# Kernel tuning notes

Hardware: AMD Instinct MI355X
Metric: run time of the kernel (lower is better)

Reference implementation:

```python
import jax, jax.numpy as jnp
import numpy as np

HEADS = 4
DIM_HEAD = 64
INNER = HEADS * DIM_HEAD  # 256
MAP_SIZE = (8, 8, 8)
DN = ('NCDHW', 'OIDHW', 'NCDHW')


def _depthwise3d(x, w):
    # x: [B,C,D,H,W], w: [C,1,3,3,3] (torch groups=C layout)
    return jax.lax.conv_general_dilated(
        x, w, window_strides=(1, 1, 1), padding='SAME',
        dimension_numbers=DN, feature_group_count=x.shape[1])


def _dws_conv(x, dw, pw):
    # depthwise 3x3x3 then pointwise 1x1x1 (pw: [out,in])
    y = _depthwise3d(x, dw)
    return jnp.einsum('bcdhw,oc->bodhw', y, pw)


def _split_heads(t):
    # 'b (dim_head heads) d h w -> b heads (d h w) dim_head'
    B, C, D, H, W = t.shape
    t = t.reshape(B, DIM_HEAD, HEADS, D * H * W)
    return t.transpose(0, 2, 3, 1)


def _merge_heads(t, D, H, W):
    # 'b heads n dim_head -> b (dim_head heads) d h w'
    B = t.shape[0]
    return t.transpose(0, 3, 1, 2).reshape(B, DIM_HEAD * HEADS, D, H, W)


def setup_inputs() -> dict:
    key = jax.random.key(0)
    ks = jax.random.split(key, 8)
    B, feat_dim, map_dim, out_dim = 2, 128, 64, 128
    D = H = W = 24
    s = 0.02
    return {
        'feat': jax.random.normal(ks[0], (B, feat_dim, D, H, W), jnp.float32),
        'smap': jax.random.normal(ks[1], (B, map_dim) + MAP_SIZE, jnp.float32),
        'feat_qv_dw': jax.random.normal(ks[2], (feat_dim, 1, 3, 3, 3), jnp.float32) * s,
        'feat_qv_pw': jax.random.normal(ks[3], (2 * INNER, feat_dim), jnp.float32) * s,
        'feat_out_dw': jax.random.normal(ks[4], (INNER, 1, 3, 3, 3), jnp.float32) * s,
        'feat_out_pw': jax.random.normal(ks[5], (out_dim, INNER), jnp.float32) * s,
        'map_qv_w': jax.random.normal(ks[6], (2 * INNER, map_dim), jnp.float32) * s,
        'map_out_w': jax.random.normal(ks[7], (map_dim, INNER), jnp.float32) * s,
    }


def reference(feat, smap, feat_qv_dw, feat_qv_pw, feat_out_dw, feat_out_pw,
              map_qv_w, map_out_w):
    B, C, D, H, W = feat.shape
    scale = DIM_HEAD ** -0.5

    # projections
    fqv = _dws_conv(feat, feat_qv_dw, feat_qv_pw)           # [B, 2*inner, D,H,W]
    feat_q, feat_v = jnp.split(fqv, 2, axis=1)
    mqv = jnp.einsum('bcdhw,oc->bodhw', smap, map_qv_w)     # [B, 2*inner, 8,8,8]
    map_q, map_v = jnp.split(mqv, 2, axis=1)

    feat_q, feat_v = _split_heads(feat_q), _split_heads(feat_v)  # [B,h,N,dh]
    map_q, map_v = _split_heads(map_q), _split_heads(map_v)      # [B,h,M,dh]

    # shared scores, dual-direction softmax
    attn = jnp.einsum('bhid,bhjd->bhij', feat_q, map_q) * scale  # [B,h,N,M]
    feat_map_attn = jax.nn.softmax(attn, axis=-1)
    map_feat_attn = jax.nn.softmax(attn, axis=-2)

    feat_out = jnp.einsum('bhij,bhjd->bhid', feat_map_attn, map_v)   # [B,h,N,dh]
    map_out = jnp.einsum('bhji,bhjd->bhid', map_feat_attn, feat_v)   # [B,h,M,dh]

    feat_out = _merge_heads(feat_out, D, H, W)
    map_out = _merge_heads(map_out, *MAP_SIZE)

    feat_out = _dws_conv(feat_out, feat_out_dw, feat_out_pw)   # [B,out_dim,D,H,W]
    map_out = jnp.einsum('bcdhw,oc->bodhw', map_out, map_out_w)  # [B,map_dim,8,8,8]
    return feat_out, map_out
```

## Files before the change

### kernel.cpp

```cpp
#include <hip/hip_runtime.h>

#define BB 2
#define CH_FEAT 128
#define HEADS 4
#define DH 64
#define INNER 256
#define NPOS 13824
#define MPOS 512
#define DSZ 24
#define JSPLIT 12
#define JCHUNK (NPOS / JSPLIT)

typedef __attribute__((ext_vector_type(8))) short bf16x8;
typedef __attribute__((ext_vector_type(4))) float f32x4;

__device__ inline unsigned short bf16_rn(float x) {
  unsigned u = __builtin_bit_cast(unsigned, x);
  u += 0x7FFF + ((u >> 16) & 1);
  return (unsigned short)(u >> 16);
}
__device__ inline unsigned pk_bf16(float a, float b) {
  return (unsigned)bf16_rn(a) | ((unsigned)bf16_rn(b) << 16);
}
__device__ inline float4 ld_bf4(const unsigned short* p) {
  uint2 u = *(const uint2*)p;
  float4 f;
  f.x = __builtin_bit_cast(float, (u.x & 0xFFFFu) << 16);
  f.y = __builtin_bit_cast(float, u.x & 0xFFFF0000u);
  f.z = __builtin_bit_cast(float, (u.y & 0xFFFFu) << 16);
  f.w = __builtin_bit_cast(float, u.y & 0xFFFF0000u);
  return f;
}
__device__ inline void st_bf4(unsigned short* p, float4 v) {
  uint2 u;
  u.x = pk_bf16(v.x, v.y);
  u.y = pk_bf16(v.z, v.w);
  *(uint2*)p = u;
}

#define GL2LDS(g, l)                                                        \
  __builtin_amdgcn_global_load_lds(                                         \
      (const __attribute__((address_space(1))) void*)(g),                   \
      (__attribute__((address_space(3))) void*)(l), 16, 0, 0)

__device__ inline bf16x8 lds_frag(const char* tile, int row, int colb) {
  return *(const bf16x8*)(tile + row * 128 + (colb ^ ((row & 7) << 4)));
}
__device__ inline bf16x8 lds_fragP(const char* tile, int row, int colb, int pitch) {
  return *(const bf16x8*)(tile + row * pitch + (colb ^ ((row & 7) << 4)));
}

__global__ __launch_bounds__(512) void k_map_qv(const float* __restrict__ smap,
                                                const float* __restrict__ w,
                                                unsigned short* __restrict__ mapqb,
                                                unsigned short* __restrict__ mapvTb) {
  int bm = blockIdx.x;
  int b = bm >> 9, m = bm & 511;
  __shared__ float s[64];
  int t = threadIdx.x;
  if (t < 64) s[t] = smap[(size_t)(b * 64 + t) * MPOS + m];
  __syncthreads();
  const float* wr = w + t * 64;
  float acc = 0.f;
#pragma unroll
  for (int c = 0; c < 64; ++c) acc += wr[c] * s[c];
  int qv = t >> 8, c2 = t & 255, head = c2 & 3, dh = c2 >> 2;
  int bh = b * HEADS + head;
  if (qv == 0)
    mapqb[((size_t)bh * MPOS + m) * 64 + dh] = bf16_rn(acc * 0.125f);
  else
    mapvTb[((size_t)bh * 64 + dh) * MPOS + m] = bf16_rn(acc);
}

__global__ __launch_bounds__(576) void k_dw_f2b(const float* __restrict__ in,
                                                const float* __restrict__ w,
                                                unsigned short* __restrict__ out, int C) {
  int t = threadIdx.x;
  int bc = blockIdx.x;
  int c = bc & (C - 1), b = bc / C;
  int y = t % 24, z = t / 24;
  const float* wr = w + c * 27;
  const float* ip = in + (size_t)bc * NPOS;

  float wm[9][3];
  int off[9];
#pragma unroll
  for (int dz = 0; dz < 3; ++dz)
#pragma unroll
    for (int dy = 0; dy < 3; ++dy) {
      int r = dz * 3 + dy;
      int zz = z + dz - 1, yy = y + dy - 1;
      float m = ((unsigned)zz < 24u && (unsigned)yy < 24u) ? 1.f : 0.f;
      wm[r][0] = wr[dz * 9 + dy * 3 + 0] * m;
      wm[r][1] = wr[dz * 9 + dy * 3 + 1] * m;
      wm[r][2] = wr[dz * 9 + dy * 3 + 2] * m;
      int zc = min(max(zz, 0), 23), yc = min(max(yy, 0), 23);
      off[r] = (zc * 24 + yc) * 24;
    }

  float4 cur[9], nxt[9];
  float pl[9];
#pragma unroll
  for (int r = 0; r < 9; ++r) {
    pl[r] = 0.f;
    cur[r] = *(const float4*)(ip + off[r]);
    nxt[r] = *(const float4*)(ip + off[r] + 4);
  }

  unsigned short* op = out + ((size_t)b * C + c) * NPOS + (z * 24 + y) * 24;
#pragma unroll
  for (int xc = 0; xc < 6; ++xc) {
    float4 acc;
    acc.x = acc.y = acc.z = acc.w = 0.f;
#pragma unroll
    for (int r = 0; r < 9; ++r) {
      float w0 = wm[r][0], w1 = wm[r][1], w2 = wm[r][2];
      float4 cu = cur[r];
      acc.x += w0 * pl[r] + w1 * cu.x + w2 * cu.y;
      acc.y += w0 * cu.x + w1 * cu.y + w2 * cu.z;
      acc.z += w0 * cu.y + w1 * cu.z + w2 * cu.w;
      acc.w += w0 * cu.z + w1 * cu.w + w2 * nxt[r].x;
    }
    st_bf4(op + xc * 4, acc);
    if (xc < 5) {
#pragma unroll
      for (int r = 0; r < 9; ++r) {
        pl[r] = cur[r].w;
        cur[r] = nxt[r];
        nxt[r] = (xc < 4) ? *(const float4*)(ip + off[r] + (xc + 2) * 4)
                          : make_float4(0.f, 0.f, 0.f, 0.f);
      }
    }
  }
}

__global__ __launch_bounds__(576) void k_dw_b2b(const unsigned short* __restrict__ in,
                                                const float* __restrict__ w,
                                                unsigned short* __restrict__ out, int C) {
  int t = threadIdx.x;
  int bc = blockIdx.x;
  int c = bc & (C - 1), b = bc / C;
  int cm = (c & 63) * 4 + (c >> 6);
  int y = t % 24, z = t / 24;
  const float* wr = w + cm * 27;
  const unsigned short* ip = in + (size_t)bc * NPOS;

  float wm[9][3];
  int off[9];
#pragma unroll
  for (int dz = 0; dz < 3; ++dz)
#pragma unroll
    for (int dy = 0; dy < 3; ++dy) {
      int r = dz * 3 + dy;
      int zz = z + dz - 1, yy = y + dy - 1;
      float m = ((unsigned)zz < 24u && (unsigned)yy < 24u) ? 1.f : 0.f;
      wm[r][0] = wr[dz * 9 + dy * 3 + 0] * m;
      wm[r][1] = wr[dz * 9 + dy * 3 + 1] * m;
      wm[r][2] = wr[dz * 9 + dy * 3 + 2] * m;
      int zc = min(max(zz, 0), 23), yc = min(max(yy, 0), 23);
      off[r] = (zc * 24 + yc) * 24;
    }

  float4 cur[9], nxt[9];
  float pl[9];
#pragma unroll
  for (int r = 0; r < 9; ++r) {
    pl[r] = 0.f;
    cur[r] = ld_bf4(ip + off[r]);
    nxt[r] = ld_bf4(ip + off[r] + 4);
  }

  unsigned short* op = out + ((size_t)b * C + cm) * NPOS + (z * 24 + y) * 24;
#pragma unroll
  for (int xc = 0; xc < 6; ++xc) {
    float4 acc;
    acc.x = acc.y = acc.z = acc.w = 0.f;
#pragma unroll
    for (int r = 0; r < 9; ++r) {
      float w0 = wm[r][0], w1 = wm[r][1], w2 = wm[r][2];
      float4 cu = cur[r];
      acc.x += w0 * pl[r] + w1 * cu.x + w2 * cu.y;
      acc.y += w0 * cu.x + w1 * cu.y + w2 * cu.z;
      acc.z += w0 * cu.y + w1 * cu.z + w2 * cu.w;
      acc.w += w0 * cu.z + w1 * cu.w + w2 * nxt[r].x;
    }
    st_bf4(op + xc * 4, acc);
    if (xc < 5) {
#pragma unroll
      for (int r = 0; r < 9; ++r) {
        pl[r] = cur[r].w;
        cur[r] = nxt[r];
        nxt[r] = (xc < 4) ? ld_bf4(ip + off[r] + (xc + 2) * 4)
                          : make_float4(0.f, 0.f, 0.f, 0.f);
      }
    }
  }
}

__global__ __launch_bounds__(256) void k_trb(const unsigned short* __restrict__ in,
                                             unsigned short* __restrict__ outT, int C) {
  __shared__ unsigned sT[64][33];
  int t = threadIdx.x;
  int n0 = blockIdx.x * 64, c0 = blockIdx.y * 64, b = blockIdx.z;
  {
    int r = t >> 2, s8 = (t & 3) * 8;
    const unsigned short* ip = in + ((size_t)b * C + c0 + r) * NPOS + n0 + s8 * 2;
    uint4 a = *(const uint4*)(ip);
    uint4 b2 = *(const uint4*)(ip + 8);
    sT[r][s8 + 0] = a.x; sT[r][s8 + 1] = a.y; sT[r][s8 + 2] = a.z; sT[r][s8 + 3] = a.w;
    sT[r][s8 + 4] = b2.x; sT[r][s8 + 5] = b2.y; sT[r][s8 + 6] = b2.z; sT[r][s8 + 7] = b2.w;
  }
  __syncthreads();
  int nr = t >> 2, cs = (t & 3) * 16;
  int n2 = nr >> 1, nl = (nr & 1) * 16;
  unsigned pkv[8];
#pragma unroll
  for (int i = 0; i < 8; ++i) {
    unsigned lo = (sT[cs + 2 * i][n2] >> nl) & 0xFFFFu;
    unsigned hi = (sT[cs + 2 * i + 1][n2] >> nl) & 0xFFFFu;
    pkv[i] = lo | (hi << 16);
  }
  unsigned short* op = outT + ((size_t)b * NPOS + n0 + nr) * C + c0 + cs;
  *(uint4*)(op) = *(uint4*)&pkv[0];
  *(uint4*)(op + 8) = *(uint4*)&pkv[4];
}

__global__ __launch_bounds__(256) void k_pwqv_m(const unsigned short* __restrict__ dwtT,
                                                const float* __restrict__ pw,
                                                unsigned short* __restrict__ fqb,
                                                unsigned short* __restrict__ fvTb) {
  __shared__ __align__(16) char sAB[49152];
  char* sW = sAB;
  char* sB = sAB + 16384;
  int t = threadIdx.x, wave = t >> 6, lane = t & 63, g = lane >> 4, c = lane & 15;
  int n0 = blockIdx.x * 128, ti = blockIdx.y, b = blockIdx.z;
  int qv = ti >> 2, head = ti & 3, bh = b * 4 + head;

  {
    int r = t >> 2, ks = (t & 3) * 32;
    int co = qv * 256 + r * 4 + head;
    const float* wp = pw + (size_t)co * 128 + ks;
    unsigned pkv[16];
#pragma unroll
    for (int i = 0; i < 8; ++i) {
      float4 v = *(const float4*)(wp + i * 4);
      pkv[2 * i] = pk_bf16(v.x, v.y);
      pkv[2 * i + 1] = pk_bf16(v.z, v.w);
    }
#pragma unroll
    for (int u = 0; u < 4; ++u) {
      int colb = (ks * 2 + u * 16) ^ ((r & 7) << 4);
      *(uint4*)(sW + r * 256 + colb) = *(uint4*)&pkv[u * 4];
    }
  }
  const char* Bg = (const char*)(dwtT + ((size_t)b * NPOS + n0) * 128);
#pragma unroll
  for (int p = 0; p < 8; ++p) {
    int oo = p * 4096 + t * 16;
    int row = oo >> 8, col = (oo & 255) ^ (((oo >> 8) & 7) << 4);
    GL2LDS(Bg + (size_t)row * 256 + col, sB + oo);
  }
  __syncthreads();

  f32x4 acc[4][2];
#pragma unroll
  for (int ct = 0; ct < 4; ++ct)
#pragma unroll
    for (int jf = 0; jf < 2; ++jf) acc[ct][jf] = (f32x4){0.f, 0.f, 0.f, 0.f};
  int nw = wave * 32;
#pragma unroll
  for (int kc = 0; kc < 4; ++kc) {
    bf16x8 bq[2];
#pragma unroll
    for (int jf = 0; jf < 2; ++jf)
      bq[jf] = lds_fragP(sB, nw + jf * 16 + c, kc * 64 + g * 16, 256);
#pragma unroll
    for (int ct = 0; ct < 4; ++ct) {
      bf16x8 a = lds_fragP(sW, ct * 16 + c, kc * 64 + g * 16, 256);
#pragma unroll
      for (int jf = 0; jf < 2; ++jf)
        acc[ct][jf] = __builtin_amdgcn_mfma_f32_16x16x32_bf16(a, bq[jf], acc[ct][jf], 0, 0, 0);
    }
  }
  __syncthreads();

  char* dmp = sB;
#pragma unroll
  for (int ct = 0; ct < 4; ++ct)
#pragma unroll
    for (int jf = 0; jf < 2; ++jf) {
      int n = nw + jf * 16 + c;
      uint2 wv;
      wv.x = pk_bf16(acc[ct][jf][0], acc[ct][jf][1]);
      wv.y = pk_bf16(acc[ct][jf][2], acc[ct][jf][3]);
      *(uint2*)(dmp + n * 144 + (ct * 16 + 4 * g) * 2) = wv;
    }
  __syncthreads();

  if (qv == 0) {
    int nr = t >> 1, seg = t & 1;
    const char* src = dmp + nr * 144 + seg * 64;
    unsigned short* dst = fqb + ((size_t)bh * NPOS + n0 + nr) * 64 + seg * 32;
#pragma unroll
    for (int i = 0; i < 4; ++i)
      *(uint4*)(dst + i * 8) = *(const uint4*)(src + i * 16);
  } else {
#pragma unroll
    for (int it = 0; it < 2; ++it) {
      int idx = it * 256 + t;
      int dh = idx >> 3, nseg = (idx & 7) * 16;
      unsigned pkv[8];
#pragma unroll
      for (int i = 0; i < 8; ++i) {
        unsigned short lo = *(const unsigned short*)(dmp + (nseg + 2 * i) * 144 + dh * 2);
        unsigned short hi = *(const unsigned short*)(dmp + (nseg + 2 * i + 1) * 144 + dh * 2);
        pkv[i] = (unsigned)lo | ((unsigned)hi << 16);
      }
      unsigned short* dst = fvTb + ((size_t)bh * 64 + dh) * NPOS + n0 + nseg;
      *(uint4*)(dst) = *(uint4*)&pkv[0];
      *(uint4*)(dst + 8) = *(uint4*)&pkv[4];
    }
  }
}

__global__ __launch_bounds__(256) void k_pwout_m(const unsigned short* __restrict__ dwoT,
                                                 const float* __restrict__ pw,
                                                 float* __restrict__ out1) {
  __shared__ __align__(16) char sW[32768];
  __shared__ __align__(16) char sB[32768];
  int t = threadIdx.x, wave = t >> 6, lane = t & 63, g = lane >> 4, c = lane & 15;
  int n0 = blockIdx.x * 128, ti = blockIdx.y, b = blockIdx.z;

  {
    int r = t >> 2, ks = (t & 3) * 64;
    const float* wp = pw + (size_t)(ti * 64 + r) * 256 + ks;
    unsigned pkv[32];
#pragma unroll
    for (int i = 0; i < 16; ++i) {
      float4 v = *(const float4*)(wp + i * 4);
      pkv[2 * i] = pk_bf16(v.x, v.y);
      pkv[2 * i + 1] = pk_bf16(v.z, v.w);
    }
#pragma unroll
    for (int u = 0; u < 8; ++u) {
      int colb = (ks * 2 + u * 16) ^ ((r & 7) << 4);
      *(uint4*)(sW + r * 512 + colb) = *(uint4*)&pkv[u * 4];
    }
  }

  f32x4 acc[4][2];
#pragma unroll
  for (int ct = 0; ct < 4; ++ct)
#pragma unroll
    for (int jf = 0; jf < 2; ++jf) acc[ct][jf] = (f32x4){0.f, 0.f, 0.f, 0.f};
  int nw = wave * 32;
  const char* Bg = (const char*)(dwoT + ((size_t)b * NPOS + n0) * 256);

  for (int kh = 0; kh < 2; ++kh) {
#pragma unroll
    for (int p = 0; p < 8; ++p) {
      int oo = p * 4096 + t * 16;
      int row = oo >> 8, col = (oo & 255) ^ (((oo >> 8) & 7) << 4);
      GL2LDS(Bg + (size_t)row * 512 + kh * 256 + col, sB + oo);
    }
    __syncthreads();
#pragma unroll
    for (int kc = 0; kc < 4; ++kc) {
      bf16x8 bq[2];
#pragma unroll
      for (int jf = 0; jf < 2; ++jf)
        bq[jf] = lds_fragP(sB, nw + jf * 16 + c, kc * 64 + g * 16, 256);
#pragma unroll
      for (int ct = 0; ct < 4; ++ct) {
        bf16x8 a = lds_fragP(sW, ct * 16 + c, (kh * 4 + kc) * 64 + g * 16, 512);
#pragma unroll
        for (int jf = 0; jf < 2; ++jf)
          acc[ct][jf] = __builtin_amdgcn_mfma_f32_16x16x32_bf16(a, bq[jf], acc[ct][jf], 0, 0, 0);
      }
    }
    __syncthreads();
  }
#pragma unroll
  for (int ct = 0; ct < 4; ++ct)
#pragma unroll
    for (int jf = 0; jf < 2; ++jf) {
      int n = n0 + nw + jf * 16 + c;
#pragma unroll
      for (int r = 0; r < 4; ++r) {
        int co = ti * 64 + ct * 16 + 4 * g + r;
        out1[((size_t)b * 128 + co) * NPOS + n] = acc[ct][jf][r];
      }
    }
}

__global__ __launch_bounds__(256) void k_attn_row(const unsigned short* __restrict__ fqb,
                                                  const unsigned short* __restrict__ mapqb,
                                                  const unsigned short* __restrict__ mapvTb,
                                                  unsigned short* __restrict__ F) {
  __shared__ __align__(16) char sK[2][8192];
  __shared__ __align__(16) char sV[2][8192];
  __shared__ __align__(16) unsigned sP[4][2][16][36];
  __shared__ float sL[4][2][16];
  int t = threadIdx.x, wave = t >> 6, lane = t & 63, g = lane >> 4, c = lane & 15;
  int bh = blockIdx.y;
  int j0 = blockIdx.x * 128 + wave * 32;

  const char* Kg = (const char*)(mapqb + (size_t)bh * MPOS * 64);
  const char* Vg = (const char*)(mapvTb + (size_t)bh * 64 * MPOS);

  const unsigned short* fqp = fqb + ((size_t)bh * NPOS + j0 + c) * 64 + 8 * g;
  bf16x8 bq00 = *(const bf16x8*)(fqp);
  bf16x8 bq01 = *(const bf16x8*)(fqp + 32);
  bf16x8 bq10 = *(const bf16x8*)(fqp + 16 * 64);
  bf16x8 bq11 = *(const bf16x8*)(fqp + 16 * 64 + 32);

  f32x4 o[2][4];
#pragma unroll
  for (int jf = 0; jf < 2; ++jf)
#pragma unroll
    for (int dt = 0; dt < 4; ++dt) o[jf][dt] = (f32x4){0.f, 0.f, 0.f, 0.f};
  float ls0 = 0.f, ls1 = 0.f;

#pragma unroll
  for (int p = 0; p < 2; ++p) {
    int oo = p * 4096 + t * 16;
    int row = oo >> 7, col = (oo & 127) ^ (((oo >> 7) & 7) << 4);
    GL2LDS(Kg + (size_t)row * 128 + col, sK[0] + oo);
    GL2LDS(Vg + (size_t)row * 1024 + col, sV[0] + oo);
  }
  __syncthreads();

  for (int ic = 0; ic < 8; ++ic) {
    const char* Kt = sK[ic & 1];
    const char* Vt = sV[ic & 1];
    if (ic < 7) {
      int ibase = (ic + 1) * 64;
#pragma unroll
      for (int p = 0; p < 2; ++p) {
        int oo = p * 4096 + t * 16;
        int row = oo >> 7, col = (oo & 127) ^ (((oo >> 7) & 7) << 4);
        GL2LDS(Kg + (size_t)(ibase + row) * 128 + col, sK[(ic + 1) & 1] + oo);
        GL2LDS(Vg + (size_t)row * 1024 + ibase * 2 + col, sV[(ic + 1) & 1] + oo);
      }
    }
#pragma unroll
    for (int ti = 0; ti < 4; ++ti) {
      bf16x8 a0 = lds_frag(Kt, ti * 16 + c, 16 * g);
      bf16x8 a1 = lds_frag(Kt, ti * 16 + c, 64 + 16 * g);
      f32x4 s0 = {0.f, 0.f, 0.f, 0.f}, s1 = {0.f, 0.f, 0.f, 0.f};
      s0 = __builtin_amdgcn_mfma_f32_16x16x32_bf16(a0, bq00, s0, 0, 0, 0);
      s0 = __builtin_amdgcn_mfma_f32_16x16x32_bf16(a1, bq01, s0, 0, 0, 0);
      s1 = __builtin_amdgcn_mfma_f32_16x16x32_bf16(a0, bq10, s1, 0, 0, 0);
      s1 = __builtin_amdgcn_mfma_f32_16x16x32_bf16(a1, bq11, s1, 0, 0, 0);
      float p0 = __expf(s0[0]), p1 = __expf(s0[1]), p2 = __expf(s0[2]), p3 = __expf(s0[3]);
      ls0 += (p0 + p1) + (p2 + p3);
      sP[wave][0][c][ti * 8 + 2 * g] = pk_bf16(p0, p1);
      sP[wave][0][c][ti * 8 + 2 * g + 1] = pk_bf16(p2, p3);
      float q0 = __expf(s1[0]), q1 = __expf(s1[1]), q2 = __expf(s1[2]), q3 = __expf(s1[3]);
      ls1 += (q0 + q1) + (q2 + q3);
      sP[wave][1][c][ti * 8 + 2 * g] = pk_bf16(q0, q1);
      sP[wave][1][c][ti * 8 + 2 * g + 1] = pk_bf16(q2, q3);
    }
#pragma unroll
    for (int ks = 0; ks < 2; ++ks) {
      bf16x8 ap0 = *(const bf16x8*)&sP[wave][0][c][ks * 16 + 4 * g];
      bf16x8 ap1 = *(const bf16x8*)&sP[wave][1][c][ks * 16 + 4 * g];
#pragma unroll
      for (int dt = 0; dt < 4; ++dt) {
        bf16x8 bv = lds_frag(Vt, dt * 16 + c, ks * 64 + 16 * g);
        o[0][dt] = __builtin_amdgcn_mfma_f32_16x16x32_bf16(ap0, bv, o[0][dt], 0, 0, 0);
        o[1][dt] = __builtin_amdgcn_mfma_f32_16x16x32_bf16(ap1, bv, o[1][dt], 0, 0, 0);
      }
    }
    __syncthreads();
  }

  ls0 += __shfl_xor(ls0, 16); ls0 += __shfl_xor(ls0, 32);
  ls1 += __shfl_xor(ls1, 16); ls1 += __shfl_xor(ls1, 32);
  if (g == 0) { sL[wave][0][c] = 1.f / ls0; sL[wave][1][c] = 1.f / ls1; }
  int b = bh >> 2, head = bh & 3;
#pragma unroll
  for (int jf = 0; jf < 2; ++jf) {
    float rl0 = sL[wave][jf][4 * g + 0], rl1 = sL[wave][jf][4 * g + 1];
    float rl2 = sL[wave][jf][4 * g + 2], rl3 = sL[wave][jf][4 * g + 3];
#pragma unroll
    for (int dt = 0; dt < 4; ++dt) {
      uint2 wv;
      wv.x = pk_bf16(o[jf][dt][0] * rl0, o[jf][dt][1] * rl1);
      wv.y = pk_bf16(o[jf][dt][2] * rl2, o[jf][dt][3] * rl3);
      *(uint2*)(F + ((size_t)b * INNER + head * 64 + dt * 16 + c) * NPOS +
                j0 + jf * 16 + 4 * g) = wv;
    }
  }
}

__global__ __launch_bounds__(256) void k_attn_col(const unsigned short* __restrict__ fqb,
                                                  const unsigned short* __restrict__ fvTb,
                                                  const unsigned short* __restrict__ mapqb,
                                                  float* __restrict__ Gc,
                                                  float* __restrict__ Gl) {
  __shared__ __align__(16) char sQ[2][8192];
  __shared__ __align__(16) char sV[2][8192];
  __shared__ __align__(16) unsigned sP[4][2][16][36];
  int t = threadIdx.x, wave = t >> 6, lane = t & 63, g = lane >> 4, c = lane & 15;
  int bh = blockIdx.y, chunk = blockIdx.z;
  int i0 = blockIdx.x * 128 + wave * 32;
  int jb = chunk * JCHUNK;

  const char* Qg = (const char*)(fqb + (size_t)bh * NPOS * 64);
  const char* Vg = (const char*)(fvTb + (size_t)bh * 64 * NPOS);

  const unsigned short* kp = mapqb + ((size_t)bh * MPOS + i0 + c) * 64 + 8 * g;
  bf16x8 bm00 = *(const bf16x8*)(kp);
  bf16x8 bm01 = *(const bf16x8*)(kp + 32);
  bf16x8 bm10 = *(const bf16x8*)(kp + 16 * 64);
  bf16x8 bm11 = *(const bf16x8*)(kp + 16 * 64 + 32);

  f32x4 o[2][4];
#pragma unroll
  for (int f = 0; f < 2; ++f)
#pragma unroll
    for (int dt = 0; dt < 4; ++dt) o[f][dt] = (f32x4){0.f, 0.f, 0.f, 0.f};
  float lc0 = 0.f, lc1 = 0.f;

#pragma unroll
  for (int p = 0; p < 2; ++p) {
    int oo = p * 4096 + t * 16;
    int row = oo >> 7, col = (oo & 127) ^ (((oo >> 7) & 7) << 4);
    GL2LDS(Qg + (size_t)(jb + row) * 128 + col, sQ[0] + oo);
    GL2LDS(Vg + (size_t)row * (NPOS * 2) + jb * 2 + col, sV[0] + oo);
  }
  __syncthreads();

  for (int jc = 0; jc < JCHUNK / 64; ++jc) {
    const char* Qt = sQ[jc & 1];
    const char* Vt = sV[jc & 1];
    if (jc < JCHUNK / 64 - 1) {
      int jbase = jb + (jc + 1) * 64;
#pragma unroll
      for (int p = 0; p < 2; ++p) {
        int oo = p * 4096 + t * 16;
        int row = oo >> 7, col = (oo & 127) ^ (((oo >> 7) & 7) << 4);
        GL2LDS(Qg + (size_t)(jbase + row) * 128 + col, sQ[(jc + 1) & 1] + oo);
        GL2LDS(Vg + (size_t)row * (NPOS * 2) + jbase * 2 + col, sV[(jc + 1) & 1] + oo);
      }
    }
#pragma unroll
    for (int tj = 0; tj < 4; ++tj) {
      bf16x8 a0 = lds_frag(Qt, tj * 16 + c, 16 * g);
      bf16x8 a1 = lds_frag(Qt, tj * 16 + c, 64 + 16 * g);
      f32x4 s0 = {0.f, 0.f, 0.f, 0.f}, s1 = {0.f, 0.f, 0.f, 0.f};
      s0 = __builtin_amdgcn_mfma_f32_16x16x32_bf16(a0, bm00, s0, 0, 0, 0);
      s0 = __builtin_amdgcn_mfma_f32_16x16x32_bf16(a1, bm01, s0, 0, 0, 0);
      s1 = __builtin_amdgcn_mfma_f32_16x16x32_bf16(a0, bm10, s1, 0, 0, 0);
      s1 = __builtin_amdgcn_mfma_f32_16x16x32_bf16(a1, bm11, s1, 0, 0, 0);
      float p0 = __expf(s0[0]), p1 = __expf(s0[1]), p2 = __expf(s0[2]), p3 = __expf(s0[3]);
      lc0 += (p0 + p1) + (p2 + p3);
      sP[wave][0][c][tj * 8 + 2 * g] = pk_bf16(p0, p1);
      sP[wave][0][c][tj * 8 + 2 * g + 1] = pk_bf16(p2, p3);
      float q0 = __expf(s1[0]), q1 = __expf(s1[1]), q2 = __expf(s1[2]), q3 = __expf(s1[3]);
      lc1 += (q0 + q1) + (q2 + q3);
      sP[wave][1][c][tj * 8 + 2 * g] = pk_bf16(q0, q1);
      sP[wave][1][c][tj * 8 + 2 * g + 1] = pk_bf16(q2, q3);
    }
#pragma unroll
    for (int ks = 0; ks < 2; ++ks) {
      bf16x8 ap0 = *(const bf16x8*)&sP[wave][0][c][ks * 16 + 4 * g];
      bf16x8 ap1 = *(const bf16x8*)&sP[wave][1][c][ks * 16 + 4 * g];
#pragma unroll
      for (int dt = 0; dt < 4; ++dt) {
        bf16x8 bv = lds_frag(Vt, dt * 16 + c, ks * 64 + 16 * g);
        o[0][dt] = __builtin_amdgcn_mfma_f32_16x16x32_bf16(ap0, bv, o[0][dt], 0, 0, 0);
        o[1][dt] = __builtin_amdgcn_mfma_f32_16x16x32_bf16(ap1, bv, o[1][dt], 0, 0, 0);
      }
    }
    __syncthreads();
  }

  lc0 += __shfl_xor(lc0, 16); lc0 += __shfl_xor(lc0, 32);
  lc1 += __shfl_xor(lc1, 16); lc1 += __shfl_xor(lc1, 32);
  int gi = chunk * 8 + bh;
  if (g == 0) {
    Gl[(size_t)gi * MPOS + i0 + c] = lc0;
    Gl[(size_t)gi * MPOS + i0 + 16 + c] = lc1;
  }
  float* gp = Gc + ((size_t)gi * MPOS + i0) * 64;
#pragma unroll
  for (int f = 0; f < 2; ++f)
#pragma unroll
    for (int dt = 0; dt < 4; ++dt)
#pragma unroll
      for (int r = 0; r < 4; ++r)
        gp[(size_t)(f * 16 + 4 * g + r) * 64 + dt * 16 + c] = o[f][dt][r];
}

__global__ __launch_bounds__(256) void k_map_out(const float* __restrict__ Gc,
                                                 const float* __restrict__ Gl,
                                                 const float* __restrict__ mow,
                                                 float* __restrict__ out2) {
  int m = blockIdx.x, b = blockIdx.y, t = threadIdx.x;
  __shared__ float sMA[256];
  __shared__ float sL[4];
  if (t < 4) {
    float l = 0.f;
#pragma unroll 4
    for (int ch = 0; ch < JSPLIT; ++ch) l += Gl[(size_t)(ch * 8 + b * 4 + t) * MPOS + m];
    sL[t] = 1.f / l;
  }
  __syncthreads();
  {
    int head = t & 3, dh = t >> 2;
    int bh = b * 4 + head;
    float a = 0.f;
#pragma unroll 4
    for (int ch = 0; ch < JSPLIT; ++ch)
      a += Gc[((size_t)(ch * 8 + bh) * MPOS + m) * 64 + dh];
    sMA[t] = a * sL[head];
  }
  __syncthreads();
  if (t < 64) {
    const float* wr = mow + t * 256;
    float acc = 0.f;
#pragma unroll 4
    for (int c = 0; c < 256; ++c) acc += wr[c] * sMA[c];
    out2[((size_t)b * 64 + t) * MPOS + m] = acc;
  }
}

extern "C" void kernel_launch(void* const* d_in, const int* in_sizes, int n_in,
                              void* d_out, int out_size, void* d_ws, size_t ws_size,
                              hipStream_t stream) {
  const float* feat = (const float*)d_in[0];
  const float* smap = (const float*)d_in[1];
  const float* fqv_dw = (const float*)d_in[2];
  const float* fqv_pw = (const float*)d_in[3];
  const float* fout_dw = (const float*)d_in[4];
  const float* fout_pw = (const float*)d_in[5];
  const float* mqv_w = (const float*)d_in[6];
  const float* mout_w = (const float*)d_in[7];

  float* out = (float*)d_out;
  float* out1 = out;
  float* out2 = out + (size_t)BB * 128 * NPOS;

  const size_t QV = (size_t)BB * HEADS * NPOS * DH;
  const size_t MQV = (size_t)BB * HEADS * MPOS * DH;
  float* ws = (float*)d_ws;
  unsigned short* F = (unsigned short*)ws;
  unsigned short* fqb = (unsigned short*)(ws + QV);
  unsigned short* fvTb = fqb + QV;
  unsigned short* mapqb = fvTb + QV;
  unsigned short* mapvTb = mapqb + MQV;
  float* Gc = (float*)(mapvTb + MQV);
  float* Gl = Gc + (size_t)JSPLIT * 8 * MPOS * 64;

  unsigned short* dwt = (unsigned short*)out1;
  unsigned short* dwtT = (unsigned short*)Gc;
  unsigned short* dwt2 = fqb;
  unsigned short* dwoT = (unsigned short*)ws;

  k_map_qv<<<dim3(BB * MPOS), dim3(512), 0, stream>>>(smap, mqv_w, mapqb, mapvTb);
  k_dw_f2b<<<dim3(BB * CH_FEAT), dim3(576), 0, stream>>>(feat, fqv_dw, dwt, CH_FEAT);
  k_trb<<<dim3(NPOS / 64, CH_FEAT / 64, BB), dim3(256), 0, stream>>>(dwt, dwtT, CH_FEAT);
  k_pwqv_m<<<dim3(NPOS / 128, 8, BB), dim3(256), 0, stream>>>(dwtT, fqv_pw, fqb, fvTb);
  k_attn_row<<<dim3(NPOS / 128, BB * HEADS), dim3(256), 0, stream>>>(fqb, mapqb, mapvTb, F);
  k_attn_col<<<dim3(MPOS / 128, BB * HEADS, JSPLIT), dim3(256), 0, stream>>>(fqb, fvTb, mapqb, Gc, Gl);
  k_map_out<<<dim3(MPOS, BB), dim3(256), 0, stream>>>(Gc, Gl, mout_w, out2);
  k_dw_b2b<<<dim3(BB * INNER), dim3(576), 0, stream>>>(F, fout_dw, dwt2, INNER);
  k_trb<<<dim3(NPOS / 64, INNER / 64, BB), dim3(256), 0, stream>>>(dwt2, dwoT, INNER);
  k_pwout_m<<<dim3(NPOS / 128, 2, BB), dim3(256), 0, stream>>>(dwoT, fout_pw, out1);
}
```

Before: 205.8 us.

## Parallelize depthwise convs per 8-wide segment, stage attn_row output via LDS, swap attn_col grid order

Both depthwise 3D conv kernels are rewritten so each thread computes one 8-wide x segment instead of a whole 24-wide row. This gives three times more threads and blocks in a flat 256-thread grid, aiming for better occupancy and shorter serial chains. k_attn_row now reuses its K/V LDS pool to stage the output tile and writes F with coalesced 16-byte row stores instead of scattered 8-byte stores. k_attn_col's grid puts the batch-head index in x, so blocks sharing the same j-chunk of Q/V are scheduled together for cache reuse. The trade-offs are redundant halo loads per segment and an extra barrier in attn_row.

```diff
diff --git a/kernel.cpp b/kernel.cpp
--- a/kernel.cpp
+++ b/kernel.cpp
@@ -22,6 +22,9 @@
 __device__ inline unsigned pk_bf16(float a, float b) {
   return (unsigned)bf16_rn(a) | ((unsigned)bf16_rn(b) << 16);
 }
+__device__ inline float bf2f(unsigned short u) {
+  return __builtin_bit_cast(float, (unsigned)u << 16);
+}
 __device__ inline float4 ld_bf4(const unsigned short* p) {
   uint2 u = *(const uint2*)p;
   float4 f;
@@ -30,12 +33,6 @@
   f.z = __builtin_bit_cast(float, (u.y & 0xFFFFu) << 16);
   f.w = __builtin_bit_cast(float, u.y & 0xFFFF0000u);
   return f;
-}
-__device__ inline void st_bf4(unsigned short* p, float4 v) {
-  uint2 u;
-  u.x = pk_bf16(v.x, v.y);
-  u.y = pk_bf16(v.z, v.w);
-  *(uint2*)p = u;
 }
 
 #define GL2LDS(g, l)                                                        \
@@ -72,129 +69,99 @@
     mapvTb[((size_t)bh * 64 + dh) * MPOS + m] = bf16_rn(acc);
 }
 
-__global__ __launch_bounds__(576) void k_dw_f2b(const float* __restrict__ in,
-                                                const float* __restrict__ w,
-                                                unsigned short* __restrict__ out, int C) {
-  int t = threadIdx.x;
-  int bc = blockIdx.x;
-  int c = bc & (C - 1), b = bc / C;
-  int y = t % 24, z = t / 24;
+__global__ __launch_bounds__(256) void k_dwf(const float* __restrict__ in,
+                                             const float* __restrict__ w,
+                                             unsigned short* __restrict__ out, int C) {
+  int tid = blockIdx.x * 256 + threadIdx.x;
+  int bc = tid / 1728;
+  int s = tid - bc * 1728;
+  int c = bc & (C - 1);
+  int xs = (s % 3) * 8;
+  int row = s / 3;
+  int y = row % 24, z = row / 24;
   const float* wr = w + c * 27;
   const float* ip = in + (size_t)bc * NPOS;
 
-  float wm[9][3];
-  int off[9];
-#pragma unroll
-  for (int dz = 0; dz < 3; ++dz)
+  float acc[8];
+#pragma unroll
+  for (int i = 0; i < 8; ++i) acc[i] = 0.f;
+
+#pragma unroll
+  for (int dz = 0; dz < 3; ++dz) {
 #pragma unroll
     for (int dy = 0; dy < 3; ++dy) {
-      int r = dz * 3 + dy;
       int zz = z + dz - 1, yy = y + dy - 1;
-      float m = ((unsigned)zz < 24u && (unsigned)yy < 24u) ? 1.f : 0.f;
-      wm[r][0] = wr[dz * 9 + dy * 3 + 0] * m;
-      wm[r][1] = wr[dz * 9 + dy * 3 + 1] * m;
-      wm[r][2] = wr[dz * 9 + dy * 3 + 2] * m;
+      bool ok = ((unsigned)zz < 24u) && ((unsigned)yy < 24u);
+      float w0 = ok ? wr[dz * 9 + dy * 3 + 0] : 0.f;
+      float w1 = ok ? wr[dz * 9 + dy * 3 + 1] : 0.f;
+      float w2 = ok ? wr[dz * 9 + dy * 3 + 2] : 0.f;
       int zc = min(max(zz, 0), 23), yc = min(max(yy, 0), 23);
-      off[r] = (zc * 24 + yc) * 24;
-    }
-
-  float4 cur[9], nxt[9];
-  float pl[9];
-#pragma unroll
-  for (int r = 0; r < 9; ++r) {
-    pl[r] = 0.f;
-    cur[r] = *(const float4*)(ip + off[r]);
-    nxt[r] = *(const float4*)(ip + off[r] + 4);
-  }
-
-  unsigned short* op = out + ((size_t)b * C + c) * NPOS + (z * 24 + y) * 24;
-#pragma unroll
-  for (int xc = 0; xc < 6; ++xc) {
-    float4 acc;
-    acc.x = acc.y = acc.z = acc.w = 0.f;
-#pragma unroll
-    for (int r = 0; r < 9; ++r) {
-      float w0 = wm[r][0], w1 = wm[r][1], w2 = wm[r][2];
-      float4 cu = cur[r];
-      acc.x += w0 * pl[r] + w1 * cu.x + w2 * cu.y;
-      acc.y += w0 * cu.x + w1 * cu.y + w2 * cu.z;
-      acc.z += w0 * cu.y + w1 * cu.z + w2 * cu.w;
-      acc.w += w0 * cu.z + w1 * cu.w + w2 * nxt[r].x;
-    }
-    st_bf4(op + xc * 4, acc);
-    if (xc < 5) {
-#pragma unroll
-      for (int r = 0; r < 9; ++r) {
-        pl[r] = cur[r].w;
-        cur[r] = nxt[r];
-        nxt[r] = (xc < 4) ? *(const float4*)(ip + off[r] + (xc + 2) * 4)
-                          : make_float4(0.f, 0.f, 0.f, 0.f);
-      }
-    }
-  }
-}
-
-__global__ __launch_bounds__(576) void k_dw_b2b(const unsigned short* __restrict__ in,
-                                                const float* __restrict__ w,
-                                                unsigned short* __restrict__ out, int C) {
-  int t = threadIdx.x;
-  int bc = blockIdx.x;
+      int ro = (zc * 24 + yc) * 24;
+      float4 Bv = *(const float4*)(ip + ro + xs);
+      float4 Cv = *(const float4*)(ip + ro + xs + 4);
+      float xm1 = xs ? *(ip + ro + xs - 1) : 0.f;
+      float x8 = (xs < 16) ? *(ip + ro + xs + 8) : 0.f;
+      float xv[10] = {xm1, Bv.x, Bv.y, Bv.z, Bv.w, Cv.x, Cv.y, Cv.z, Cv.w, x8};
+#pragma unroll
+      for (int i = 0; i < 8; ++i)
+        acc[i] += w0 * xv[i] + w1 * xv[i + 1] + w2 * xv[i + 2];
+    }
+  }
+  unsigned short* op = out + (size_t)bc * NPOS + row * 24 + xs;
+  uint4 pv;
+  pv.x = pk_bf16(acc[0], acc[1]);
+  pv.y = pk_bf16(acc[2], acc[3]);
+  pv.z = pk_bf16(acc[4], acc[5]);
+  pv.w = pk_bf16(acc[6], acc[7]);
+  *(uint4*)op = pv;
+}
+
+__global__ __launch_bounds__(256) void k_dwb(const unsigned short* __restrict__ in,
+                                             const float* __restrict__ w,
+                                             unsigned short* __restrict__ out, int C) {
+  int tid = blockIdx.x * 256 + threadIdx.x;
+  int bc = tid / 1728;
+  int s = tid - bc * 1728;
   int c = bc & (C - 1), b = bc / C;
   int cm = (c & 63) * 4 + (c >> 6);
-  int y = t % 24, z = t / 24;
+  int xs = (s % 3) * 8;
+  int row = s / 3;
+  int y = row % 24, z = row / 24;
   const float* wr = w + cm * 27;
   const unsigned short* ip = in + (size_t)bc * NPOS;
 
-  float wm[9][3];
-  int off[9];
-#pragma unroll
-  for (int dz = 0; dz < 3; ++dz)
+  float acc[8];
+#pragma unroll
+  for (int i = 0; i < 8; ++i) acc[i] = 0.f;
+
+#pragma unroll
+  for (int dz = 0; dz < 3; ++dz) {
 #pragma unroll
     for (int dy = 0; dy < 3; ++dy) {
-      int r = dz * 3 + dy;
       int zz = z + dz - 1, yy = y + dy - 1;
-      float m = ((unsigned)zz < 24u && (unsigned)yy < 24u) ? 1.f : 0.f;
-      wm[r][0] = wr[dz * 9 + dy * 3 + 0] * m;
-      wm[r][1] = wr[dz * 9 + dy * 3 + 1] * m;
-      wm[r][2] = wr[dz * 9 + dy * 3 + 2] * m;
+      bool ok = ((unsigned)zz < 24u) && ((unsigned)yy < 24u);
+      float w0 = ok ? wr[dz * 9 + dy * 3 + 0] : 0.f;
+      float w1 = ok ? wr[dz * 9 + dy * 3 + 1] : 0.f;
+      float w2 = ok ? wr[dz * 9 + dy * 3 + 2] : 0.f;
       int zc = min(max(zz, 0), 23), yc = min(max(yy, 0), 23);
-      off[r] = (zc * 24 + yc) * 24;
-    }
-
-  float4 cur[9], nxt[9];
-  float pl[9];
-#pragma unroll
-  for (int r = 0; r < 9; ++r) {
-    pl[r] = 0.f;
-    cur[r] = ld_bf4(ip + off[r]);
-    nxt[r] = ld_bf4(ip + off[r] + 4);
-  }
-
-  unsigned short* op = out + ((size_t)b * C + cm) * NPOS + (z * 24 + y) * 24;
-#pragma unroll
-  for (int xc = 0; xc < 6; ++xc) {
-    float4 acc;
-    acc.x = acc.y = acc.z = acc.w = 0.f;
-#pragma unroll
-    for (int r = 0; r < 9; ++r) {
-      float w0 = wm[r][0], w1 = wm[r][1], w2 = wm[r][2];
-      float4 cu = cur[r];
-      acc.x += w0 * pl[r] + w1 * cu.x + w2 * cu.y;
-      acc.y += w0 * cu.x + w1 * cu.y + w2 * cu.z;
-      acc.z += w0 * cu.y + w1 * cu.z + w2 * cu.w;
-      acc.w += w0 * cu.z + w1 * cu.w + w2 * nxt[r].x;
-    }
-    st_bf4(op + xc * 4, acc);
-    if (xc < 5) {
-#pragma unroll
-      for (int r = 0; r < 9; ++r) {
-        pl[r] = cur[r].w;
-        cur[r] = nxt[r];
-        nxt[r] = (xc < 4) ? ld_bf4(ip + off[r] + (xc + 2) * 4)
-                          : make_float4(0.f, 0.f, 0.f, 0.f);
-      }
-    }
-  }
+      int ro = (zc * 24 + yc) * 24;
+      float4 Bv = ld_bf4(ip + ro + xs);
+      float4 Cv = ld_bf4(ip + ro + xs + 4);
+      float xm1 = xs ? bf2f(ip[ro + xs - 1]) : 0.f;
+      float x8 = (xs < 16) ? bf2f(ip[ro + xs + 8]) : 0.f;
+      float xv[10] = {xm1, Bv.x, Bv.y, Bv.z, Bv.w, Cv.x, Cv.y, Cv.z, Cv.w, x8};
+#pragma unroll
+      for (int i = 0; i < 8; ++i)
+        acc[i] += w0 * xv[i] + w1 * xv[i + 1] + w2 * xv[i + 2];
+    }
+  }
+  unsigned short* op = out + ((size_t)b * C + cm) * NPOS + row * 24 + xs;
+  uint4 pv;
+  pv.x = pk_bf16(acc[0], acc[1]);
+  pv.y = pk_bf16(acc[2], acc[3]);
+  pv.z = pk_bf16(acc[4], acc[5]);
+  pv.w = pk_bf16(acc[6], acc[7]);
+  *(uint4*)op = pv;
 }
 
 __global__ __launch_bounds__(256) void k_trb(const unsigned short* __restrict__ in,
@@ -397,8 +364,7 @@
                                                   const unsigned short* __restrict__ mapqb,
                                                   const unsigned short* __restrict__ mapvTb,
                                                   unsigned short* __restrict__ F) {
-  __shared__ __align__(16) char sK[2][8192];
-  __shared__ __align__(16) char sV[2][8192];
+  __shared__ __align__(16) char sPool[32768];
   __shared__ __align__(16) unsigned sP[4][2][16][36];
   __shared__ float sL[4][2][16];
   int t = threadIdx.x, wave = t >> 6, lane = t & 63, g = lane >> 4, c = lane & 15;
@@ -425,22 +391,23 @@
   for (int p = 0; p < 2; ++p) {
     int oo = p * 4096 + t * 16;
     int row = oo >> 7, col = (oo & 127) ^ (((oo >> 7) & 7) << 4);
-    GL2LDS(Kg + (size_t)row * 128 + col, sK[0] + oo);
-    GL2LDS(Vg + (size_t)row * 1024 + col, sV[0] + oo);
+    GL2LDS(Kg + (size_t)row * 128 + col, sPool + oo);
+    GL2LDS(Vg + (size_t)row * 1024 + col, sPool + 16384 + oo);
   }
   __syncthreads();
 
   for (int ic = 0; ic < 8; ++ic) {
-    const char* Kt = sK[ic & 1];
-    const char* Vt = sV[ic & 1];
+    const char* Kt = sPool + (ic & 1) * 8192;
+    const char* Vt = sPool + 16384 + (ic & 1) * 8192;
     if (ic < 7) {
       int ibase = (ic + 1) * 64;
+      int bsel = ((ic + 1) & 1) * 8192;
 #pragma unroll
       for (int p = 0; p < 2; ++p) {
         int oo = p * 4096 + t * 16;
         int row = oo >> 7, col = (oo & 127) ^ (((oo >> 7) & 7) << 4);
-        GL2LDS(Kg + (size_t)(ibase + row) * 128 + col, sK[(ic + 1) & 1] + oo);
-        GL2LDS(Vg + (size_t)row * 1024 + ibase * 2 + col, sV[(ic + 1) & 1] + oo);
+        GL2LDS(Kg + (size_t)(ibase + row) * 128 + col, sPool + bsel + oo);
+        GL2LDS(Vg + (size_t)row * 1024 + ibase * 2 + col, sPool + 16384 + bsel + oo);
       }
     }
 #pragma unroll
@@ -478,7 +445,6 @@
   ls0 += __shfl_xor(ls0, 16); ls0 += __shfl_xor(ls0, 32);
   ls1 += __shfl_xor(ls1, 16); ls1 += __shfl_xor(ls1, 32);
   if (g == 0) { sL[wave][0][c] = 1.f / ls0; sL[wave][1][c] = 1.f / ls1; }
-  int b = bh >> 2, head = bh & 3;
 #pragma unroll
   for (int jf = 0; jf < 2; ++jf) {
     float rl0 = sL[wave][jf][4 * g + 0], rl1 = sL[wave][jf][4 * g + 1];
@@ -488,9 +454,19 @@
       uint2 wv;
       wv.x = pk_bf16(o[jf][dt][0] * rl0, o[jf][dt][1] * rl1);
       wv.y = pk_bf16(o[jf][dt][2] * rl2, o[jf][dt][3] * rl3);
-      *(uint2*)(F + ((size_t)b * INNER + head * 64 + dt * 16 + c) * NPOS +
-                j0 + jf * 16 + 4 * g) = wv;
-    }
+      *(uint2*)(sPool + (dt * 16 + c) * 272 + (wave * 32 + jf * 16 + 4 * g) * 2) = wv;
+    }
+  }
+  __syncthreads();
+  {
+    int ch = t >> 2, seg = t & 3;
+    int b = bh >> 2, head = bh & 3;
+    unsigned short* dst = F + ((size_t)b * INNER + head * 64 + ch) * NPOS +
+                          blockIdx.x * 128 + seg * 32;
+    const char* src = sPool + ch * 272 + seg * 64;
+#pragma unroll
+    for (int i = 0; i < 4; ++i)
+      *(uint4*)(dst + i * 8) = *(const uint4*)(src + i * 16);
   }
 }
 
@@ -503,8 +479,8 @@
   __shared__ __align__(16) char sV[2][8192];
   __shared__ __align__(16) unsigned sP[4][2][16][36];
   int t = threadIdx.x, wave = t >> 6, lane = t & 63, g = lane >> 4, c = lane & 15;
-  int bh = blockIdx.y, chunk = blockIdx.z;
-  int i0 = blockIdx.x * 128 + wave * 32;
+  int bh = blockIdx.x, chunk = blockIdx.z;
+  int i0 = blockIdx.y * 128 + wave * 32;
   int jb = chunk * JCHUNK;
 
   const char* Qg = (const char*)(fqb + (size_t)bh * NPOS * 64);
@@ -660,13 +636,13 @@
   unsigned short* dwoT = (unsigned short*)ws;
 
   k_map_qv<<<dim3(BB * MPOS), dim3(512), 0, stream>>>(smap, mqv_w, mapqb, mapvTb);
-  k_dw_f2b<<<dim3(BB * CH_FEAT), dim3(576), 0, stream>>>(feat, fqv_dw, dwt, CH_FEAT);
+  k_dwf<<<dim3(BB * CH_FEAT * 1728 / 256), dim3(256), 0, stream>>>(feat, fqv_dw, dwt, CH_FEAT);
   k_trb<<<dim3(NPOS / 64, CH_FEAT / 64, BB), dim3(256), 0, stream>>>(dwt, dwtT, CH_FEAT);
   k_pwqv_m<<<dim3(NPOS / 128, 8, BB), dim3(256), 0, stream>>>(dwtT, fqv_pw, fqb, fvTb);
   k_attn_row<<<dim3(NPOS / 128, BB * HEADS), dim3(256), 0, stream>>>(fqb, mapqb, mapvTb, F);
-  k_attn_col<<<dim3(MPOS / 128, BB * HEADS, JSPLIT), dim3(256), 0, stream>>>(fqb, fvTb, mapqb, Gc, Gl);
+  k_attn_col<<<dim3(8, MPOS / 128, JSPLIT), dim3(256), 0, stream>>>(fqb, fvTb, mapqb, Gc, Gl);
   k_map_out<<<dim3(MPOS, BB), dim3(256), 0, stream>>>(Gc, Gl, mout_w, out2);
-  k_dw_b2b<<<dim3(BB * INNER), dim3(576), 0, stream>>>(F, fout_dw, dwt2, INNER);
+  k_dwb<<<dim3(BB * INNER * 1728 / 256), dim3(256), 0, stream>>>(F, fout_dw, dwt2, INNER);
   k_trb<<<dim3(NPOS / 64, INNER / 64, BB), dim3(256), 0, stream>>>(dwt2, dwoT, INNER);
   k_pwout_m<<<dim3(NPOS / 128, 2, BB), dim3(256), 0, stream>>>(dwoT, fout_pw, out1);
 }
```

Result: no change. 205.5 us (-0.1%).
